# Kernel tuning notes

Hardware: AMD Instinct MI355X
Metric: run time of the kernel (lower is better)

Reference implementation:

```python
import jax, jax.numpy as jnp
import numpy as np

# Layer widths of the fixed ClassicPINN stack: 3 -> 8x7 -> 16x3 -> 32x3 -> 16 -> 3
WIDTHS = [3, 8, 8, 8, 8, 8, 8, 8, 16, 16, 16, 32, 32, 32, 16, 3]
N_LAYERS = 15
OUT_SIZES = [1, 1, 1]
N_POINTS = 1048576


def setup_inputs() -> dict:
    key = jax.random.key(0)
    ks = jax.random.split(key, 1 + 2 * N_LAYERS)
    inp = {"coords": jax.random.normal(ks[0], (N_POINTS, WIDTHS[0]), dtype=jnp.float32)}
    # PyTorch nn.Linear default init: U(-1/sqrt(fan_in), 1/sqrt(fan_in)) for W and b
    for i in range(N_LAYERS):
        fan_in, fan_out = WIDTHS[i], WIDTHS[i + 1]
        bound = 1.0 / np.sqrt(fan_in)
        inp[f"W{i}"] = jax.random.uniform(ks[1 + 2 * i], (fan_out, fan_in), jnp.float32, -bound, bound)
        inp[f"b{i}"] = jax.random.uniform(ks[2 + 2 * i], (fan_out,), jnp.float32, -bound, bound)
    return inp


def reference(coords, W0, W1, W2, W3, W4, W5, W6, W7, W8, W9, W10, W11, W12, W13, W14,
              b0, b1, b2, b3, b4, b5, b6, b7, b8, b9, b10, b11, b12, b13, b14):
    Ws = [W0, W1, W2, W3, W4, W5, W6, W7, W8, W9, W10, W11, W12, W13, W14]
    bs = [b0, b1, b2, b3, b4, b5, b6, b7, b8, b9, b10, b11, b12, b13, b14]
    h = coords  # [N, 3]
    for i in range(N_LAYERS):
        h = h @ Ws[i].T + bs[i]
        if i < N_LAYERS - 1:  # Tanh after every layer except the last
            h = jnp.tanh(h)
    # torch.split(output, [1,1,1], dim=1)
    return (h[:, 0:1], h[:, 1:2], h[:, 2:3])
```

## Files before the change

kernel.cpp:

```cpp
#include <hip/hip_runtime.h>


#define NPTS 1048576
#define P 2

typedef float f32x2 __attribute__((ext_vector_type(2)));

struct PinnParams {
    const float* W[15];
    const float* B[15];
};

__constant__ constexpr int kIN[15]   = {3, 8, 8, 8, 8, 8, 8, 8, 16, 16, 16, 32, 32, 32, 16};
__constant__ constexpr int kOUT[15]  = {8, 8, 8, 8, 8, 8, 8, 16, 16, 16, 32, 32, 32, 16, 3};
__constant__ constexpr int kWSZ[15]  = {24, 64, 64, 64, 64, 64, 64, 128, 256, 256, 512, 1024, 1024, 512, 48};
__constant__ constexpr int kWOFF[15] = {0, 24, 88, 152, 216, 280, 344, 408, 536, 792, 1048, 1560, 2584, 3608, 4120};
__constant__ constexpr int kBOFF[15] = {0, 8, 16, 24, 32, 40, 48, 56, 72, 88, 104, 136, 168, 200, 216};
#define WTOT 4168
#define BTOT 219

__device__ __forceinline__ float fast_tanh(float x) {
    x = __builtin_amdgcn_fmed3f(x, -9.5f, 9.5f);
    float e = __builtin_amdgcn_exp2f(x * 2.8853900817779268f);
    return 1.0f - 2.0f * __builtin_amdgcn_rcpf(e + 1.0f);
}

__device__ __forceinline__ f32x2 tanh2(f32x2 x) {
    return f32x2{fast_tanh(x.x), fast_tanh(x.y)};
}

template <int L, bool TANH>
__device__ __forceinline__ void layerL(const float* __restrict__ ldsw,
                                       const float* __restrict__ ldsb,
                                       const f32x2* h, f32x2* o) {
    constexpr int IN = kIN[L], OUT = kOUT[L], WO = kWOFF[L], BO = kBOFF[L];
    static_assert(IN % 4 == 0, "use layer0 for IN=3");
#pragma unroll
    for (int j = 0; j < OUT; ++j) {
        const float b = ldsb[BO + j];
        f32x2 acc = {b, b};
#pragma unroll
        for (int k = 0; k < IN; k += 4) {
            const float4 w = *reinterpret_cast<const float4*>(ldsw + WO + j * IN + k);
            acc = __builtin_elementwise_fma(f32x2{w.x, w.x}, h[k + 0], acc);
            acc = __builtin_elementwise_fma(f32x2{w.y, w.y}, h[k + 1], acc);
            acc = __builtin_elementwise_fma(f32x2{w.z, w.z}, h[k + 2], acc);
            acc = __builtin_elementwise_fma(f32x2{w.w, w.w}, h[k + 3], acc);
        }
        o[j] = TANH ? tanh2(acc) : acc;
    }
}

__device__ __forceinline__ void layer0(const float* __restrict__ ldsw,
                                       const float* __restrict__ ldsb,
                                       const f32x2* h, f32x2* o) {
#pragma unroll
    for (int j = 0; j < 8; ++j) {
        const float w0 = ldsw[3 * j], w1 = ldsw[3 * j + 1], w2 = ldsw[3 * j + 2];
        const float b = ldsb[j];
        f32x2 acc = {b, b};
        acc = __builtin_elementwise_fma(f32x2{w0, w0}, h[0], acc);
        acc = __builtin_elementwise_fma(f32x2{w1, w1}, h[1], acc);
        acc = __builtin_elementwise_fma(f32x2{w2, w2}, h[2], acc);
        o[j] = tanh2(acc);
    }
}

__global__ __launch_bounds__(256, 2) void pinn_fwd(const float* __restrict__ coords,
                                                   PinnParams prm,
                                                   float* __restrict__ out) {
    __shared__ __align__(16) float ldsw[WTOT];
    __shared__ float ldsb[BTOT];

    const int tid = threadIdx.x;
#pragma unroll
    for (int l = 0; l < 15; ++l) {
        const float* __restrict__ W = prm.W[l];
        for (int idx = tid; idx < kWSZ[l]; idx += 256) ldsw[kWOFF[l] + idx] = W[idx];
        const float* __restrict__ B = prm.B[l];
        if (tid < kOUT[l]) ldsb[kBOFF[l] + tid] = B[tid];
    }
    __syncthreads();

    const int t = blockIdx.x * 256 + tid;
    const int i0 = t * P;
    const f32x2* cp = reinterpret_cast<const f32x2*>(coords + 3 * i0);
    const f32x2 q0 = cp[0], q1 = cp[1], q2 = cp[2];

    f32x2 a[32], c[32];
    a[0] = f32x2{q0.x, q1.y};
    a[1] = f32x2{q0.y, q2.x};
    a[2] = f32x2{q1.x, q2.y};

    layer0(ldsw, ldsb, a, c);
    layerL<1, true>(ldsw, ldsb, c, a);
    layerL<2, true>(ldsw, ldsb, a, c);
    layerL<3, true>(ldsw, ldsb, c, a);
    layerL<4, true>(ldsw, ldsb, a, c);
    layerL<5, true>(ldsw, ldsb, c, a);
    layerL<6, true>(ldsw, ldsb, a, c);
    layerL<7, true>(ldsw, ldsb, c, a);
    layerL<8, true>(ldsw, ldsb, a, c);
    layerL<9, true>(ldsw, ldsb, c, a);
    layerL<10, true>(ldsw, ldsb, a, c);
    layerL<11, true>(ldsw, ldsb, c, a);
    layerL<12, true>(ldsw, ldsb, a, c);
    layerL<13, true>(ldsw, ldsb, c, a);
    layerL<14, false>(ldsw, ldsb, a, c);

    *reinterpret_cast<f32x2*>(out + i0) = c[0];
    *reinterpret_cast<f32x2*>(out + NPTS + i0) = c[1];
    *reinterpret_cast<f32x2*>(out + 2 * NPTS + i0) = c[2];
}

extern "C" void kernel_launch(void* const* d_in, const int* in_sizes, int n_in,
                              void* d_out, int out_size, void* d_ws, size_t ws_size,
                              hipStream_t stream) {
    const float* coords = (const float*)d_in[0];
    PinnParams prm;
    for (int l = 0; l < 15; ++l) {
        prm.W[l] = (const float*)d_in[1 + 2 * l];
        prm.B[l] = (const float*)d_in[2 + 2 * l];
    }
    pinn_fwd<<<NPTS / (256 * P), 256, 0, stream>>>(coords, prm, (float*)d_out);
}
```

Measured before the change: 275.5 us.

## Transpose weights in LDS and pack output neurons into f32x2 FMAs, one point per thread

Weights are stored transposed in shared memory so each input activation is broadcast against pairs of output-neuron weights. This lets packed FMAs work over neighbouring output neurons instead of two points per thread. Each thread now handles a single point, the grid doubles, and launch bounds are raised to 4 blocks per CU for more occupancy. The cost is twice as many blocks each reloading and transposing the weights into LDS, plus scalar tanh and strided coordinate loads.

```diff
diff --git a/kernel.cpp b/kernel.cpp
--- a/kernel.cpp
+++ b/kernel.cpp
@@ -2,7 +2,6 @@
 
 
 #define NPTS 1048576
-#define P 2
 
 typedef float f32x2 __attribute__((ext_vector_type(2)));
 
@@ -25,92 +24,93 @@
     return 1.0f - 2.0f * __builtin_amdgcn_rcpf(e + 1.0f);
 }
 
-__device__ __forceinline__ f32x2 tanh2(f32x2 x) {
-    return f32x2{fast_tanh(x.x), fast_tanh(x.y)};
-}
-
 template <int L, bool TANH>
-__device__ __forceinline__ void layerL(const float* __restrict__ ldsw,
+__device__ __forceinline__ void layerT(const float* __restrict__ ldswT,
                                        const float* __restrict__ ldsb,
-                                       const f32x2* h, f32x2* o) {
+                                       const float* h, float* o) {
     constexpr int IN = kIN[L], OUT = kOUT[L], WO = kWOFF[L], BO = kBOFF[L];
-    static_assert(IN % 4 == 0, "use layer0 for IN=3");
+    static_assert(OUT % 4 == 0, "generic path needs OUT%4==0");
+    f32x2 acc[OUT / 2];
 #pragma unroll
-    for (int j = 0; j < OUT; ++j) {
-        const float b = ldsb[BO + j];
-        f32x2 acc = {b, b};
+    for (int j2 = 0; j2 < OUT / 2; ++j2)
+        acc[j2] = *reinterpret_cast<const f32x2*>(ldsb + BO + 2 * j2);
 #pragma unroll
-        for (int k = 0; k < IN; k += 4) {
-            const float4 w = *reinterpret_cast<const float4*>(ldsw + WO + j * IN + k);
-            acc = __builtin_elementwise_fma(f32x2{w.x, w.x}, h[k + 0], acc);
-            acc = __builtin_elementwise_fma(f32x2{w.y, w.y}, h[k + 1], acc);
-            acc = __builtin_elementwise_fma(f32x2{w.z, w.z}, h[k + 2], acc);
-            acc = __builtin_elementwise_fma(f32x2{w.w, w.w}, h[k + 3], acc);
+    for (int k = 0; k < IN; ++k) {
+        const float hk = h[k];
+        const f32x2 hb = {hk, hk};
+        const float* wrow = ldswT + WO + k * OUT;
+#pragma unroll
+        for (int j4 = 0; j4 < OUT / 4; ++j4) {
+            const float4 w = *reinterpret_cast<const float4*>(wrow + 4 * j4);
+            acc[2 * j4 + 0] = __builtin_elementwise_fma(f32x2{w.x, w.y}, hb, acc[2 * j4 + 0]);
+            acc[2 * j4 + 1] = __builtin_elementwise_fma(f32x2{w.z, w.w}, hb, acc[2 * j4 + 1]);
         }
-        o[j] = TANH ? tanh2(acc) : acc;
+    }
+#pragma unroll
+    for (int j2 = 0; j2 < OUT / 2; ++j2) {
+        o[2 * j2 + 0] = TANH ? fast_tanh(acc[j2].x) : acc[j2].x;
+        o[2 * j2 + 1] = TANH ? fast_tanh(acc[j2].y) : acc[j2].y;
     }
 }
 
-__device__ __forceinline__ void layer0(const float* __restrict__ ldsw,
-                                       const float* __restrict__ ldsb,
-                                       const f32x2* h, f32x2* o) {
+__device__ __forceinline__ void layer14(const float* __restrict__ ldswT,
+                                        const float* __restrict__ ldsb,
+                                        const float* h, float* o) {
+    constexpr int WO = kWOFF[14], BO = kBOFF[14];
+    float a0 = ldsb[BO + 0], a1 = ldsb[BO + 1], a2 = ldsb[BO + 2];
 #pragma unroll
-    for (int j = 0; j < 8; ++j) {
-        const float w0 = ldsw[3 * j], w1 = ldsw[3 * j + 1], w2 = ldsw[3 * j + 2];
-        const float b = ldsb[j];
-        f32x2 acc = {b, b};
-        acc = __builtin_elementwise_fma(f32x2{w0, w0}, h[0], acc);
-        acc = __builtin_elementwise_fma(f32x2{w1, w1}, h[1], acc);
-        acc = __builtin_elementwise_fma(f32x2{w2, w2}, h[2], acc);
-        o[j] = tanh2(acc);
+    for (int k = 0; k < 16; ++k) {
+        const float* wrow = ldswT + WO + k * 3;
+        a0 = fmaf(wrow[0], h[k], a0);
+        a1 = fmaf(wrow[1], h[k], a1);
+        a2 = fmaf(wrow[2], h[k], a2);
     }
+    o[0] = a0; o[1] = a1; o[2] = a2;
 }
 
-__global__ __launch_bounds__(256, 2) void pinn_fwd(const float* __restrict__ coords,
+__global__ __launch_bounds__(256, 4) void pinn_fwd(const float* __restrict__ coords,
                                                    PinnParams prm,
                                                    float* __restrict__ out) {
-    __shared__ __align__(16) float ldsw[WTOT];
+    __shared__ __align__(16) float ldswT[WTOT];
     __shared__ float ldsb[BTOT];
 
     const int tid = threadIdx.x;
-#pragma unroll
     for (int l = 0; l < 15; ++l) {
         const float* __restrict__ W = prm.W[l];
-        for (int idx = tid; idx < kWSZ[l]; idx += 256) ldsw[kWOFF[l] + idx] = W[idx];
-        const float* __restrict__ B = prm.B[l];
-        if (tid < kOUT[l]) ldsb[kBOFF[l] + tid] = B[tid];
+        const int IN = kIN[l], OUT = kOUT[l], WO = kWOFF[l], SZ = kWSZ[l];
+        for (int idx = tid; idx < SZ; idx += 256) {
+            const int j = idx / IN, k = idx - j * IN;
+            ldswT[WO + k * OUT + j] = W[idx];
+        }
+        if (tid < OUT) ldsb[kBOFF[l] + tid] = prm.B[l][tid];
     }
     __syncthreads();
 
     const int t = blockIdx.x * 256 + tid;
-    const int i0 = t * P;
-    const f32x2* cp = reinterpret_cast<const f32x2*>(coords + 3 * i0);
-    const f32x2 q0 = cp[0], q1 = cp[1], q2 = cp[2];
+    float a[32], c[32];
+    a[0] = coords[3 * t + 0];
+    a[1] = coords[3 * t + 1];
+    a[2] = coords[3 * t + 2];
 
-    f32x2 a[32], c[32];
-    a[0] = f32x2{q0.x, q1.y};
-    a[1] = f32x2{q0.y, q2.x};
-    a[2] = f32x2{q1.x, q2.y};
+    layerT<0, true>(ldswT, ldsb, a, c);
+    layerT<1, true>(ldswT, ldsb, c, a);
+    layerT<2, true>(ldswT, ldsb, a, c);
+    layerT<3, true>(ldswT, ldsb, c, a);
+    layerT<4, true>(ldswT, ldsb, a, c);
+    layerT<5, true>(ldswT, ldsb, c, a);
+    layerT<6, true>(ldswT, ldsb, a, c);
+    layerT<7, true>(ldswT, ldsb, c, a);
+    layerT<8, true>(ldswT, ldsb, a, c);
+    layerT<9, true>(ldswT, ldsb, c, a);
+    layerT<10, true>(ldswT, ldsb, a, c);
+    layerT<11, true>(ldswT, ldsb, c, a);
+    layerT<12, true>(ldswT, ldsb, a, c);
+    layerT<13, true>(ldswT, ldsb, c, a);
+    layer14(ldswT, ldsb, a, c);
 
-    layer0(ldsw, ldsb, a, c);
-    layerL<1, true>(ldsw, ldsb, c, a);
-    layerL<2, true>(ldsw, ldsb, a, c);
-    layerL<3, true>(ldsw, ldsb, c, a);
-    layerL<4, true>(ldsw, ldsb, a, c);
-    layerL<5, true>(ldsw, ldsb, c, a);
-    layerL<6, true>(ldsw, ldsb, a, c);
-    layerL<7, true>(ldsw, ldsb, c, a);
-    layerL<8, true>(ldsw, ldsb, a, c);
-    layerL<9, true>(ldsw, ldsb, c, a);
-    layerL<10, true>(ldsw, ldsb, a, c);
-    layerL<11, true>(ldsw, ldsb, c, a);
-    layerL<12, true>(ldsw, ldsb, a, c);
-    layerL<13, true>(ldsw, ldsb, c, a);
-    layerL<14, false>(ldsw, ldsb, a, c);
-
-    *reinterpret_cast<f32x2*>(out + i0) = c[0];
-    *reinterpret_cast<f32x2*>(out + NPTS + i0) = c[1];
-    *reinterpret_cast<f32x2*>(out + 2 * NPTS + i0) = c[2];
+    out[t] = c[0];
+    out[NPTS + t] = c[1];
+    out[2 * NPTS + t] = c[2];
 }
 
 extern "C" void kernel_launch(void* const* d_in, const int* in_sizes, int n_in,
@@ -122,5 +122,5 @@
         prm.W[l] = (const float*)d_in[1 + 2 * l];
         prm.B[l] = (const float*)d_in[2 + 2 * l];
     }
-    pinn_fwd<<<NPTS / (256 * P), 256, 0, stream>>>(coords, prm, (float*)d_out);
+    pinn_fwd<<<NPTS / 256, 256, 0, stream>>>(coords, prm, (float*)d_out);
 }
```

After: 319.0 us. 1.16x slower.
